# Kernel optimization log

Measured on AMD Instinct MI355X. Metric: run time of the kernel, lower is better.

The kernel has to match this reference:

```python
import jax, jax.numpy as jnp
import numpy as np

N = 8192
F_IN = 128
F_OUT = 64
NEG_INF = -9e15


def setup_inputs() -> dict:
    key = jax.random.key(0)
    k1, k2, k3, k4 = jax.random.split(key, 4)
    x = jax.random.normal(k1, (N, F_IN), dtype=jnp.float32)
    adj = jax.random.randint(k2, (N, N), 0, 2, dtype=jnp.int32)
    W = jax.random.normal(k3, (F_OUT, F_IN), dtype=jnp.float32) * 0.05  # torch Linear weight [out,in]
    a = jax.random.normal(k4, (1, 2 * F_OUT), dtype=jnp.float32) * 0.05  # attention vector weight [1, 2*out]
    return {"x": x, "adj": adj, "W": W, "a": a}


def reference(x, adj, W, a):
    fout = W.shape[0]
    Wh = x @ W.T                                   # [N, out]
    a1 = a[0, :fout]                               # a.weight.T[:out]
    a2 = a[0, fout:]                               # a.weight.T[out:]
    Wh1 = Wh @ a1                                  # [N]
    Wh2 = Wh @ a2                                  # [N]
    e = jax.nn.leaky_relu(Wh1[:, None] + Wh2[None, :], negative_slope=0.2)  # [N, N]
    attention = jnp.where(adj > 0, e, NEG_INF)
    attention = jax.nn.softmax(attention, axis=1)
    # dropout is identity in eval / deterministic reference
    h_prime = attention @ Wh                       # [N, out]
    return jax.nn.elu(h_prime)
```

## Files before the change

kernel.cpp:

```cpp
#include <hip/hip_runtime.h>
#include <hip/hip_bf16.h>
#include <cstdint>
#include <cstddef>

#define NN 8192
#define FIN 128
#define FOUT 64

typedef __attribute__((ext_vector_type(8))) short short8;
typedef __attribute__((ext_vector_type(4))) float f32x4;

__device__ __forceinline__ unsigned short f32_to_bf16_bits(float f) {
    union { float f; uint32_t u; } c; c.f = f;
    uint32_t u = c.u;
    u += 0x7fffu + ((u >> 16) & 1u);
    return (unsigned short)(u >> 16);
}

__global__ __launch_bounds__(256) void gat_prep(
    const float* __restrict__ x, const float* __restrict__ W,
    const float* __restrict__ a, unsigned short* __restrict__ WhT,
    float* __restrict__ Wh1, float* __restrict__ Wh2)
{
    const int t    = threadIdx.x;
    const int f    = t & 63;
    const int iloc = t >> 6;
    const int i    = blockIdx.x * 4 + iloc;

    const float4* x4 = (const float4*)(x + (size_t)i * FIN);
    const float4* w4 = (const float4*)(W + (size_t)f * FIN);

    float acc = 0.f;
#pragma unroll
    for (int k = 0; k < FIN / 4; ++k) {
        float4 xv = x4[k];
        float4 wv = w4[k];
        acc += xv.x * wv.x + xv.y * wv.y + xv.z * wv.z + xv.w * wv.w;
    }

    WhT[(size_t)f * NN + i] = f32_to_bf16_bits(acc);

    float r1 = acc * a[f];
    float r2 = acc * a[64 + f];
#pragma unroll
    for (int m = 1; m < 64; m <<= 1) {
        r1 += __shfl_xor(r1, m, 64);
        r2 += __shfl_xor(r2, m, 64);
    }
    if (f == 0) { Wh1[i] = r1; Wh2[i] = r2; }
}

__global__ __launch_bounds__(1024, 4) void gat_attn(
    const int* __restrict__ adj, const unsigned short* __restrict__ WhT,
    const float* __restrict__ Wh1, const float* __restrict__ Wh2,
    float* __restrict__ out)
{
    __shared__ float lds_C[16][32][66];
    __shared__ float lds_tot[16][32];

    const int tid  = threadIdx.x;
    const int wave = tid >> 6;
    const int lane = tid & 63;
    const int il   = lane & 15;
    const int q    = lane >> 4;
    const int i0   = blockIdx.x * 32;
    const int iA   = i0 + il;
    const int iB   = i0 + 16 + il;

    const float wh1A = Wh1[iA];
    const float wh1B = Wh1[iB];
    const int   jbase = wave * 32 + q * 8;
    const int* __restrict__ adjA = adj + (size_t)iA * NN;
    const int* __restrict__ adjB = adj + (size_t)iB * NN;

    const short8* bp0 = (const short8*)(WhT + (size_t)(0  + il) * NN);
    const short8* bp1 = (const short8*)(WhT + (size_t)(16 + il) * NN);
    const short8* bp2 = (const short8*)(WhT + (size_t)(32 + il) * NN);
    const short8* bp3 = (const short8*)(WhT + (size_t)(48 + il) * NN);

    f32x4 acc0 = {0.f, 0.f, 0.f, 0.f};
    f32x4 acc1 = {0.f, 0.f, 0.f, 0.f};
    f32x4 acc2 = {0.f, 0.f, 0.f, 0.f};
    f32x4 acc3 = {0.f, 0.f, 0.f, 0.f};
    f32x4 acc4 = {0.f, 0.f, 0.f, 0.f};
    f32x4 acc5 = {0.f, 0.f, 0.f, 0.f};
    f32x4 acc6 = {0.f, 0.f, 0.f, 0.f};
    f32x4 acc7 = {0.f, 0.f, 0.f, 0.f};
    float totA = 0.f, totB = 0.f;

    int4 avA0 = *(const int4*)(adjA + jbase);
    int4 avA1 = *(const int4*)(adjA + jbase + 4);
    int4 avB0 = *(const int4*)(adjB + jbase);
    int4 avB1 = *(const int4*)(adjB + jbase + 4);

#pragma unroll 1
    for (int tt = 0; tt < 16; ++tt) {
        const int jn = jbase + (((tt + 1) & 15) << 9);
        const int4 nA0 = *(const int4*)(adjA + jn);
        const int4 nA1 = *(const int4*)(adjA + jn + 4);
        const int4 nB0 = *(const int4*)(adjB + jn);
        const int4 nB1 = *(const int4*)(adjB + jn + 4);

        const int j  = jbase + (tt << 9);
        const float4 w20 = *(const float4*)(Wh2 + j);
        const float4 w21 = *(const float4*)(Wh2 + j + 4);
        const int jb = j >> 3;
        const short8 b0 = bp0[jb];
        const short8 b1 = bp1[jb];
        const short8 b2 = bp2[jb];
        const short8 b3 = bp3[jb];

        float wv[8];
#define CALC(idx, adjv, wh1v, wh2v, totv)                              \
        {                                                              \
            float s = (wh1v) + (wh2v);                                 \
            float e = fmaxf(s, 0.2f * s);          \
            float v = ((adjv) > 0) ? __expf(e) : 0.f;                  \
            totv += v;                                                 \
            wv[idx] = v;                                               \
        }
        CALC(0, avA0.x, wh1A, w20.x, totA) CALC(1, avA0.y, wh1A, w20.y, totA)
        CALC(2, avA0.z, wh1A, w20.z, totA) CALC(3, avA0.w, wh1A, w20.w, totA)
        CALC(4, avA1.x, wh1A, w21.x, totA) CALC(5, avA1.y, wh1A, w21.y, totA)
        CALC(6, avA1.z, wh1A, w21.z, totA) CALC(7, avA1.w, wh1A, w21.w, totA)
        union { short8 v; __hip_bfloat162 h[4]; } afA;
        afA.h[0] = __float22bfloat162_rn(float2{wv[0], wv[1]});
        afA.h[1] = __float22bfloat162_rn(float2{wv[2], wv[3]});
        afA.h[2] = __float22bfloat162_rn(float2{wv[4], wv[5]});
        afA.h[3] = __float22bfloat162_rn(float2{wv[6], wv[7]});

        CALC(0, avB0.x, wh1B, w20.x, totB) CALC(1, avB0.y, wh1B, w20.y, totB)
        CALC(2, avB0.z, wh1B, w20.z, totB) CALC(3, avB0.w, wh1B, w20.w, totB)
        CALC(4, avB1.x, wh1B, w21.x, totB) CALC(5, avB1.y, wh1B, w21.y, totB)
        CALC(6, avB1.z, wh1B, w21.z, totB) CALC(7, avB1.w, wh1B, w21.w, totB)
#undef CALC
        union { short8 v; __hip_bfloat162 h[4]; } afB;
        afB.h[0] = __float22bfloat162_rn(float2{wv[0], wv[1]});
        afB.h[1] = __float22bfloat162_rn(float2{wv[2], wv[3]});
        afB.h[2] = __float22bfloat162_rn(float2{wv[4], wv[5]});
        afB.h[3] = __float22bfloat162_rn(float2{wv[6], wv[7]});

        acc0 = __builtin_amdgcn_mfma_f32_16x16x32_bf16(afA.v, b0, acc0, 0, 0, 0);
        acc1 = __builtin_amdgcn_mfma_f32_16x16x32_bf16(afA.v, b1, acc1, 0, 0, 0);
        acc2 = __builtin_amdgcn_mfma_f32_16x16x32_bf16(afA.v, b2, acc2, 0, 0, 0);
        acc3 = __builtin_amdgcn_mfma_f32_16x16x32_bf16(afA.v, b3, acc3, 0, 0, 0);
        acc4 = __builtin_amdgcn_mfma_f32_16x16x32_bf16(afB.v, b0, acc4, 0, 0, 0);
        acc5 = __builtin_amdgcn_mfma_f32_16x16x32_bf16(afB.v, b1, acc5, 0, 0, 0);
        acc6 = __builtin_amdgcn_mfma_f32_16x16x32_bf16(afB.v, b2, acc6, 0, 0, 0);
        acc7 = __builtin_amdgcn_mfma_f32_16x16x32_bf16(afB.v, b3, acc7, 0, 0, 0);

        avA0 = nA0; avA1 = nA1; avB0 = nB0; avB1 = nB1;
    }

    totA += __shfl_xor(totA, 16, 64);
    totA += __shfl_xor(totA, 32, 64);
    totB += __shfl_xor(totB, 16, 64);
    totB += __shfl_xor(totB, 32, 64);
    if (lane < 16) {
        lds_tot[wave][lane]      = totA;
        lds_tot[wave][16 + lane] = totB;
    }

#pragma unroll
    for (int r = 0; r < 4; ++r) {
        lds_C[wave][q * 4 + r][0 * 16 + il] = acc0[r];
        lds_C[wave][q * 4 + r][1 * 16 + il] = acc1[r];
        lds_C[wave][q * 4 + r][2 * 16 + il] = acc2[r];
        lds_C[wave][q * 4 + r][3 * 16 + il] = acc3[r];
        lds_C[wave][16 + q * 4 + r][0 * 16 + il] = acc4[r];
        lds_C[wave][16 + q * 4 + r][1 * 16 + il] = acc5[r];
        lds_C[wave][16 + q * 4 + r][2 * 16 + il] = acc6[r];
        lds_C[wave][16 + q * 4 + r][3 * 16 + il] = acc7[r];
    }
    __syncthreads();

#pragma unroll
    for (int e = 0; e < 2; ++e) {
        const int idx = e * 1024 + tid;
        const int ii = idx >> 6;
        const int ff = idx & 63;
        float s = 0.f;
        float t = 0.f;
#pragma unroll
        for (int w = 0; w < 16; ++w) {
            s += lds_C[w][ii][ff];
            t += lds_tot[w][ii];
        }
        const float p = s / t;
        out[(size_t)(i0 + ii) * FOUT + ff] = (p > 0.f) ? p : (__expf(p) - 1.f);
    }
}

extern "C" void kernel_launch(void* const* d_in, const int* in_sizes, int n_in,
                              void* d_out, int out_size, void* d_ws, size_t ws_size,
                              hipStream_t stream) {
    const float* x   = (const float*)d_in[0];
    const int*   adj = (const int*)d_in[1];
    const float* W   = (const float*)d_in[2];
    const float* a   = (const float*)d_in[3];
    float* out = (float*)d_out;

    char* ws = (char*)d_ws;
    unsigned short* WhT = (unsigned short*)ws;
    float* Wh1   = (float*)(ws + (size_t)1048576);
    float* Wh2   = (float*)(ws + (size_t)1048576 + 32768);

    gat_prep<<<dim3(NN / 4), dim3(256), 0, stream>>>(x, W, a, WhT, Wh1, Wh2);
    gat_attn<<<dim3(NN / 32), dim3(1024), 0, stream>>>(adj, WhT, Wh1, Wh2, out);
}
```

Before: 425.2 us.

## Pack adjacency into bitmask in a separate pass before attention

Adds a pre-pass that reads the int32 adjacency matrix with coalesced loads and compresses it into a 64-bit-per-word bitmask using wave ballots. The attention kernel then reads one 64-bit word per row group instead of 32 bytes of ints per lane per step, and drops the adjacency prefetch registers. The aim is to replace scattered, latency-bound adjacency loads inside the compute kernel with a streaming pass. The cost is an extra kernel launch and an extra small mask write and read.

```diff
diff --git a/kernel.cpp b/kernel.cpp
--- a/kernel.cpp
+++ b/kernel.cpp
@@ -50,8 +50,24 @@
     if (f == 0) { Wh1[i] = r1; Wh2[i] = r2; }
 }
 
+__global__ __launch_bounds__(256) void gat_pack(
+    const int* __restrict__ adj, unsigned long long* __restrict__ mask)
+{
+    const int lane = threadIdx.x & 63;
+    const int wv   = (int)((blockIdx.x * 256 + threadIdx.x) >> 6);
+    const size_t w0 = (size_t)wv * 128;
+#pragma unroll 8
+    for (int k = 0; k < 128; ++k) {
+        const size_t w = w0 + k;
+        const int v = adj[w * 64 + lane];
+        const unsigned long long b = __ballot(v > 0);
+        if (lane == 0) mask[w] = b;
+    }
+}
+
 __global__ __launch_bounds__(1024, 4) void gat_attn(
-    const int* __restrict__ adj, const unsigned short* __restrict__ WhT,
+    const unsigned long long* __restrict__ mask,
+    const unsigned short* __restrict__ WhT,
     const float* __restrict__ Wh1, const float* __restrict__ Wh2,
     float* __restrict__ out)
 {
@@ -70,8 +86,10 @@
     const float wh1A = Wh1[iA];
     const float wh1B = Wh1[iB];
     const int   jbase = wave * 32 + q * 8;
-    const int* __restrict__ adjA = adj + (size_t)iA * NN;
-    const int* __restrict__ adjB = adj + (size_t)iB * NN;
+
+    const unsigned long long* __restrict__ mrowA = mask + (size_t)iA * (NN / 64);
+    const unsigned long long* __restrict__ mrowB = mask + (size_t)iB * (NN / 64);
+    const int msh = ((wave & 1) << 5) + (q << 3);
 
     const short8* bp0 = (const short8*)(WhT + (size_t)(0  + il) * NN);
     const short8* bp1 = (const short8*)(WhT + (size_t)(16 + il) * NN);
@@ -88,18 +106,11 @@
     f32x4 acc7 = {0.f, 0.f, 0.f, 0.f};
     float totA = 0.f, totB = 0.f;
 
-    int4 avA0 = *(const int4*)(adjA + jbase);
-    int4 avA1 = *(const int4*)(adjA + jbase + 4);
-    int4 avB0 = *(const int4*)(adjB + jbase);
-    int4 avB1 = *(const int4*)(adjB + jbase + 4);
-
 #pragma unroll 1
     for (int tt = 0; tt < 16; ++tt) {
-        const int jn = jbase + (((tt + 1) & 15) << 9);
-        const int4 nA0 = *(const int4*)(adjA + jn);
-        const int4 nA1 = *(const int4*)(adjA + jn + 4);
-        const int4 nB0 = *(const int4*)(adjB + jn);
-        const int4 nB1 = *(const int4*)(adjB + jn + 4);
+        const int g = (tt << 3) + (wave >> 1);
+        const unsigned int bitsA = (unsigned int)(mrowA[g] >> msh) & 0xffu;
+        const unsigned int bitsB = (unsigned int)(mrowB[g] >> msh) & 0xffu;
 
         const int j  = jbase + (tt << 9);
         const float4 w20 = *(const float4*)(Wh2 + j);
@@ -111,28 +122,28 @@
         const short8 b3 = bp3[jb];
 
         float wv[8];
-#define CALC(idx, adjv, wh1v, wh2v, totv)                              \
+#define CALC(idx, bitsv, wh1v, wh2v, totv)                             \
         {                                                              \
             float s = (wh1v) + (wh2v);                                 \
             float e = fmaxf(s, 0.2f * s);          \
-            float v = ((adjv) > 0) ? __expf(e) : 0.f;                  \
+            float v = ((bitsv >> idx) & 1u) ? __expf(e) : 0.f;         \
             totv += v;                                                 \
             wv[idx] = v;                                               \
         }
-        CALC(0, avA0.x, wh1A, w20.x, totA) CALC(1, avA0.y, wh1A, w20.y, totA)
-        CALC(2, avA0.z, wh1A, w20.z, totA) CALC(3, avA0.w, wh1A, w20.w, totA)
-        CALC(4, avA1.x, wh1A, w21.x, totA) CALC(5, avA1.y, wh1A, w21.y, totA)
-        CALC(6, avA1.z, wh1A, w21.z, totA) CALC(7, avA1.w, wh1A, w21.w, totA)
+        CALC(0, bitsA, wh1A, w20.x, totA) CALC(1, bitsA, wh1A, w20.y, totA)
+        CALC(2, bitsA, wh1A, w20.z, totA) CALC(3, bitsA, wh1A, w20.w, totA)
+        CALC(4, bitsA, wh1A, w21.x, totA) CALC(5, bitsA, wh1A, w21.y, totA)
+        CALC(6, bitsA, wh1A, w21.z, totA) CALC(7, bitsA, wh1A, w21.w, totA)
         union { short8 v; __hip_bfloat162 h[4]; } afA;
         afA.h[0] = __float22bfloat162_rn(float2{wv[0], wv[1]});
         afA.h[1] = __float22bfloat162_rn(float2{wv[2], wv[3]});
         afA.h[2] = __float22bfloat162_rn(float2{wv[4], wv[5]});
         afA.h[3] = __float22bfloat162_rn(float2{wv[6], wv[7]});
 
-        CALC(0, avB0.x, wh1B, w20.x, totB) CALC(1, avB0.y, wh1B, w20.y, totB)
-        CALC(2, avB0.z, wh1B, w20.z, totB) CALC(3, avB0.w, wh1B, w20.w, totB)
-        CALC(4, avB1.x, wh1B, w21.x, totB) CALC(5, avB1.y, wh1B, w21.y, totB)
-        CALC(6, avB1.z, wh1B, w21.z, totB) CALC(7, avB1.w, wh1B, w21.w, totB)
+        CALC(0, bitsB, wh1B, w20.x, totB) CALC(1, bitsB, wh1B, w20.y, totB)
+        CALC(2, bitsB, wh1B, w20.z, totB) CALC(3, bitsB, wh1B, w20.w, totB)
+        CALC(4, bitsB, wh1B, w21.x, totB) CALC(5, bitsB, wh1B, w21.y, totB)
+        CALC(6, bitsB, wh1B, w21.z, totB) CALC(7, bitsB, wh1B, w21.w, totB)
 #undef CALC
         union { short8 v; __hip_bfloat162 h[4]; } afB;
         afB.h[0] = __float22bfloat162_rn(float2{wv[0], wv[1]});
@@ -148,8 +159,6 @@
         acc5 = __builtin_amdgcn_mfma_f32_16x16x32_bf16(afB.v, b1, acc5, 0, 0, 0);
         acc6 = __builtin_amdgcn_mfma_f32_16x16x32_bf16(afB.v, b2, acc6, 0, 0, 0);
         acc7 = __builtin_amdgcn_mfma_f32_16x16x32_bf16(afB.v, b3, acc7, 0, 0, 0);
-
-        avA0 = nA0; avA1 = nA1; avB0 = nB0; avB1 = nB1;
     }
 
     totA += __shfl_xor(totA, 16, 64);
@@ -202,9 +211,12 @@
 
     char* ws = (char*)d_ws;
     unsigned short* WhT = (unsigned short*)ws;
-    float* Wh1   = (float*)(ws + (size_t)1048576);
-    float* Wh2   = (float*)(ws + (size_t)1048576 + 32768);
+    float* Wh1  = (float*)(ws + (size_t)1048576);
+    float* Wh2  = (float*)(ws + (size_t)1048576 + 32768);
+    unsigned long long* mask =
+        (unsigned long long*)(ws + (size_t)2097152);
 
     gat_prep<<<dim3(NN / 4), dim3(256), 0, stream>>>(x, W, a, WhT, Wh1, Wh2);
-    gat_attn<<<dim3(NN / 32), dim3(1024), 0, stream>>>(adj, WhT, Wh1, Wh2, out);
-}
+    gat_pack<<<dim3(2048), dim3(256), 0, stream>>>(adj, mask);
+    gat_attn<<<dim3(NN / 32), dim3(1024), 0, stream>>>(mask, WhT, Wh1, Wh2, out);
+}
```

New measurement: 492.1 us. +15.7%, slower.
